# Optimization experiments

Measured on AMD Instinct MI355X. Metric: run time of the kernel, lower is better.

## Reference

```python
import jax, jax.numpy as jnp
import numpy as np

# Module hyperparameters (init_kwargs)
N_CLASSES = 21
RADIUS = 5
SIZE = (256, 256)
SIGMA_DIST = 4.0
SIGMA_FEAT = 1.0
B, C = 8, 32


def _offsets(radius):
    """Integer (dy, dx) offsets with Euclidean distance < radius (includes (0,0))."""
    offs = []
    r = int(radius)
    for dy in range(-r + 1, r):
        for dx in range(-r + 1, r):
            if dy * dy + dx * dx < radius * radius:
                offs.append((dy, dx))
    return offs


OFFSETS = _offsets(RADIUS)  # 69 offsets for radius=5


def setup_inputs() -> dict:
    key = jax.random.key(0)
    k1, k2 = jax.random.split(key)
    H, W = SIZE
    classification = jax.random.uniform(k1, (B, N_CLASSES, H, W), dtype=jnp.float32)
    features = jax.random.normal(k2, (B, C, H, W), dtype=jnp.float32)
    return {"classification": classification, "features": features}


def reference(classification, features):
    # classification: [B, K, H, W] soft assignments S
    # features:       [B, C, H, W]
    Bb, K, H, W = classification.shape
    inv_sd2 = 1.0 / (SIGMA_DIST * SIGMA_DIST)
    inv_sf2 = 1.0 / (SIGMA_FEAT * SIGMA_FEAT)

    hs = jnp.arange(H)
    ws = jnp.arange(W)

    WS = jnp.zeros_like(classification)           # (W @ S), [B, K, H, W]
    degree = jnp.zeros((Bb, H, W), classification.dtype)

    # Loop over the small fixed set of neighbor offsets (69 for radius=5).
    for dy, dx in OFFSETS:
        f_nb = jnp.roll(features, (-dy, -dx), axis=(2, 3))
        s_nb = jnp.roll(classification, (-dy, -dx), axis=(2, 3))
        # mask out wrap-around: neighbor (h+dy, w+dx) must be in-bounds
        valid_h = (hs + dy >= 0) & (hs + dy < H)
        valid_w = (ws + dx >= 0) & (ws + dx < W)
        mask = (valid_h[:, None] & valid_w[None, :]).astype(classification.dtype)
        # Gaussian affinity: distance kernel * feature kernel
        feat_d2 = ((features - f_nb) ** 2).sum(axis=1)        # [B, H, W]
        w = jnp.exp(-(dy * dy + dx * dx) * inv_sd2 - feat_d2 * inv_sf2) * mask
        WS = WS + w[:, None] * s_nb
        degree = degree + w

    # numerator   = S^T W S : [B, K, K]
    # denominator = d^T S   : [B, K]
    num = jnp.einsum('bkhw,bjhw->bkj', classification, WS)
    den = jnp.einsum('bhw,bkhw->bk', degree, classification)
    return (num / den[:, None, :]).sum()
```

## Files before the change

kernel.cpp:

```cpp
#include <hip/hip_runtime.h>

#define HH 256
#define WW 256
#define HWPX 65536
#define BB 8
#define KK 21
#define CC 32
#define NT 8192
#define E_LOG2E 1.4426950408889634f
#define PEN -30000.0f

typedef _Float16 half2v __attribute__((ext_vector_type(2)));
typedef _Float16 half8  __attribute__((ext_vector_type(8)));
typedef float    f32x4v __attribute__((ext_vector_type(4)));
union F4H { float4 f4; half2v h[4]; half8 h8; };

__global__ __launch_bounds__(256) void prep(const float* __restrict__ cls,
                                            const float* __restrict__ feat,
                                            float4* __restrict__ fpk,
                                            float2* __restrict__ TN,
                                            float* __restrict__ out) {
    const int tid = blockIdx.x * 256 + threadIdx.x;
    if (tid == 0) out[0] = 0.f;
    const int b = tid >> 16;
    const int p = tid & (HWPX - 1);

    const float* cbase = cls + (size_t)b * KK * HWPX + p;
    float T = 0.f;
#pragma unroll
    for (int k = 0; k < KK; ++k) T += cbase[(size_t)k * HWPX];

    const float* src = feat + (size_t)b * CC * HWPX + p;
    float nq = 0.f;
#pragma unroll
    for (int j = 0; j < 4; ++j) {
        F4H u;
#pragma unroll
        for (int k = 0; k < 4; ++k) {
            float a  = src[(size_t)(j * 8 + 2 * k) * HWPX];
            float b2 = src[(size_t)(j * 8 + 2 * k + 1) * HWPX];
            u.h[k] = __builtin_bit_cast(half2v, __builtin_amdgcn_cvt_pkrtz(a, b2));
            nq = __builtin_amdgcn_fdot2(u.h[k], u.h[k], nq, false);
        }
        fpk[(size_t)j * (BB * HWPX) + tid] = u.f4;
    }
    TN[tid] = make_float2(T, nq);
}

__global__ __launch_bounds__(256, 6) void affinity_mfma(const float4* __restrict__ fpk,
                                                        const float2* __restrict__ TN,
                                                        const float* __restrict__ cls,
                                                        float* __restrict__ partial) {
    __shared__ float smN[4][21], smD[4][21];
    const int L    = blockIdx.x;
    const int b    = L & 7;
    const int t    = L >> 3;
    const int wid  = threadIdx.x >> 6;
    const int lane = threadIdx.x & 63;
    const int g    = lane >> 4;
    const int c    = lane & 15;
    const int idx  = t * 4 + wid;
    const int y0   = (idx >> 5) * 2;
    const int x0   = (idx & 31) * 8;

    const size_t bofs = (size_t)b * HWPX;
    const float4* fb  = fpk + bofs;
    const float2* tnb = TN + bofs;

    F4H afr;
    afr.f4 = fb[(size_t)g * (BB * HWPX) + ((y0 + (c & 1)) << 8) + x0 + (c >> 1)];

    int pxr[4];
    float npE[4];
#pragma unroll
    for (int r = 0; r < 4; ++r) {
        pxr[r] = ((y0 + (r & 1)) << 8) + x0 + 2 * g + (r >> 1);
        npE[r] = tnb[pxr[r]].y * E_LOG2E;
    }

    const int xbu  = x0 - 4 + c;
    const bool inb = (unsigned)xbu < WW;
    const int xbc  = min(max(xbu, 0), WW - 1);
    const int voffF = (g * (BB * HWPX) + xbc) * 16;
    const int voffT = xbc * 8;

    float cstL16[4], cstL9[4], cstL4[4];
#pragma unroll
    for (int r = 0; r < 4; ++r) {
        const int dx = c - 4 - 2 * g - (r >> 1);
        const int s2 = dx * dx;
        const float bp = fmaf((float)s2, -E_LOG2E / 16.f, -npE[r]);
        cstL16[r] = (inb && s2 <= 16) ? bp : PEN;
        cstL9[r]  = (inb && s2 <= 9)  ? bp : PEN;
        cstL4[r]  = (inb && s2 <= 4)  ? bp : PEN;
    }

    const f32x4v czero = {0.f, 0.f, 0.f, 0.f};
    float pdeg[4] = {0.f, 0.f, 0.f, 0.f};
    float pV[4]   = {0.f, 0.f, 0.f, 0.f};

    const char* fpkB = (const char*)fpk + bofs * 16;
    const char* tnB  = (const char*)TN + bofs * 8;

    auto body = [&](int ny, const float (&ce)[4], const float (&co)[4],
                    float cdyE, float cdyO, int mode) {
        if ((unsigned)ny >= HH) return;
        const char* pF = fpkB + ((size_t)ny << 12);
        const char* pT = tnB  + ((size_t)ny << 11);
        F4H bfr; bfr.f4 = *(const float4*)(pF + voffF);
        const float2 tq = *(const float2*)(pT + voffT);
        f32x4v cz = __builtin_amdgcn_mfma_f32_16x16x32_f16(afr.h8, bfr.h8, czero, 0, 0, 0);
        if (mode != 2) {
            const float te = fmaf(tq.y, -E_LOG2E, cdyE);
            const float e0 = fmaf(cz[0], 2.f * E_LOG2E, ce[0] + te);
            const float w0 = __builtin_exp2f(e0);
            pdeg[0] += w0;  pV[0] = fmaf(w0, tq.x, pV[0]);
            const float e2 = fmaf(cz[2], 2.f * E_LOG2E, ce[2] + te);
            const float w2 = __builtin_exp2f(e2);
            pdeg[2] += w2;  pV[2] = fmaf(w2, tq.x, pV[2]);
        }
        if (mode != 1) {
            const float to = fmaf(tq.y, -E_LOG2E, cdyO);
            const float e1 = fmaf(cz[1], 2.f * E_LOG2E, co[1] + to);
            const float w1 = __builtin_exp2f(e1);
            pdeg[1] += w1;  pV[1] = fmaf(w1, tq.x, pV[1]);
            const float e3 = fmaf(cz[3], 2.f * E_LOG2E, co[3] + to);
            const float w3 = __builtin_exp2f(e3);
            pdeg[3] += w3;  pV[3] = fmaf(w3, tq.x, pV[3]);
        }
    };

#define CDY(D) ((float)(D) * (-E_LOG2E / 16.f))
    body(y0 - 4, cstL4,  cstL4,  CDY(16), CDY(16), 1);
    body(y0 - 3, cstL9,  cstL4,  CDY(9),  CDY(16), 0);
    body(y0 - 2, cstL16, cstL9,  CDY(4),  CDY(9),  0);
    body(y0 - 1, cstL16, cstL16, CDY(1),  CDY(4),  0);
    body(y0 + 0, cstL16, cstL16, CDY(0),  CDY(1),  0);
    body(y0 + 1, cstL16, cstL16, CDY(1),  CDY(0),  0);
    body(y0 + 2, cstL16, cstL16, CDY(4),  CDY(1),  0);
    body(y0 + 3, cstL9,  cstL16, CDY(9),  CDY(4),  0);
    body(y0 + 4, cstL4,  cstL9,  CDY(16), CDY(9),  0);
    body(y0 + 5, cstL4,  cstL4,  CDY(16), CDY(16), 2);
#undef CDY

#pragma unroll
    for (int m = 1; m <= 8; m <<= 1) {
#pragma unroll
        for (int r = 0; r < 4; ++r) {
            pdeg[r] += __shfl_xor(pdeg[r], m, 64);
            pV[r]   += __shfl_xor(pV[r], m, 64);
        }
    }

    float n0 = 0.f, d0 = 0.f, n1 = 0.f, d1 = 0.f;
    const float* clsb = cls + (size_t)b * KK * HWPX;
#pragma unroll
    for (int r = 0; r < 4; ++r) {
        const float s0 = clsb[(size_t)c * HWPX + pxr[r]];
        n0 = fmaf(s0, pV[r], n0);
        d0 = fmaf(s0, pdeg[r], d0);
        if (c < 5) {
            const float s1 = clsb[(size_t)(c + 16) * HWPX + pxr[r]];
            n1 = fmaf(s1, pV[r], n1);
            d1 = fmaf(s1, pdeg[r], d1);
        }
    }
#pragma unroll
    for (int m = 16; m <= 32; m <<= 1) {
        n0 += __shfl_xor(n0, m, 64);
        d0 += __shfl_xor(d0, m, 64);
        n1 += __shfl_xor(n1, m, 64);
        d1 += __shfl_xor(d1, m, 64);
    }
    if (lane < 16) {
        smN[wid][lane] = n0;
        smD[wid][lane] = d0;
        if (lane < 5) { smN[wid][16 + lane] = n1; smD[wid][16 + lane] = d1; }
    }
    __syncthreads();
    if (threadIdx.x < 2 * KK) {
        const int jq = threadIdx.x;
        const float v = (jq < KK)
            ? (smN[0][jq] + smN[1][jq] + smN[2][jq] + smN[3][jq])
            : (smD[0][jq - KK] + smD[1][jq - KK] + smD[2][jq - KK] + smD[3][jq - KK]);
        partial[(size_t)jq * NT + (size_t)b * 1024 + t] = v;
    }
}

__global__ __launch_bounds__(256) void reduce_fin(const float* __restrict__ partial,
                                                  float* __restrict__ out) {
    __shared__ float smn[4], smd[4];
    const int j = blockIdx.x;
    const int b = blockIdx.y;
    const float4 n4 = ((const float4*)(partial + (size_t)j        * NT + (size_t)b * 1024))[threadIdx.x];
    const float4 d4 = ((const float4*)(partial + (size_t)(j + KK) * NT + (size_t)b * 1024))[threadIdx.x];
    float n = (n4.x + n4.y) + (n4.z + n4.w);
    float d = (d4.x + d4.y) + (d4.z + d4.w);
#pragma unroll
    for (int off = 32; off > 0; off >>= 1) {
        n += __shfl_down(n, off);
        d += __shfl_down(d, off);
    }
    if ((threadIdx.x & 63) == 0) { smn[threadIdx.x >> 6] = n; smd[threadIdx.x >> 6] = d; }
    __syncthreads();
    if (threadIdx.x == 0) {
        const float N = (smn[0] + smn[1]) + (smn[2] + smn[3]);
        const float D = (smd[0] + smd[1]) + (smd[2] + smd[3]);
        atomicAdd(out, N / D);
    }
}

extern "C" void kernel_launch(void* const* d_in, const int* in_sizes, int n_in,
                              void* d_out, int out_size, void* d_ws, size_t ws_size,
                              hipStream_t stream) {
    const float* cls  = (const float*)d_in[0];
    const float* feat = (const float*)d_in[1];
    float* out = (float*)d_out;

    const size_t BHW = (size_t)BB * HWPX;
    float4* fpk     = (float4*)d_ws;
    float2* TN      = (float2*)((char*)d_ws + BHW * 64);
    float*  partial = (float*)((char*)TN + BHW * 8);

    prep<<<dim3((BB * HWPX) / 256), dim3(256), 0, stream>>>(cls, feat, fpk, TN, out);
    affinity_mfma<<<dim3(NT), dim3(256), 0, stream>>>(fpk, TN, cls, partial);
    reduce_fin<<<dim3(KK, BB), dim3(256), 0, stream>>>(partial, out);
}
```

Measured before the change: 179.4 us.

## Process two row-pairs per wave to reuse neighbor-row loads across tiles

Each wave now covers 4 rows instead of 2, holding two A fragments and running 12 neighbor-row windows in place of 2×10. Each loaded neighbor row (features and T/norm) feeds MFMAs for both tiles, which cuts the global loads for the halo rows. Grid size and partial-reduction layout are halved to match. The cost is more live registers (a second set of accumulators and constants), which may lower occupancy under the 6-wave launch bound.

```diff
diff --git a/kernel.cpp b/kernel.cpp
--- a/kernel.cpp
+++ b/kernel.cpp
@@ -6,7 +6,7 @@
 #define BB 8
 #define KK 21
 #define CC 32
-#define NT 8192
+#define NTB 4096
 #define E_LOG2E 1.4426950408889634f
 #define PEN -30000.0f
 
@@ -60,22 +60,24 @@
     const int g    = lane >> 4;
     const int c    = lane & 15;
     const int idx  = t * 4 + wid;
-    const int y0   = (idx >> 5) * 2;
+    const int y0   = (idx >> 5) * 4;
     const int x0   = (idx & 31) * 8;
 
     const size_t bofs = (size_t)b * HWPX;
     const float4* fb  = fpk + bofs;
     const float2* tnb = TN + bofs;
 
-    F4H afr;
-    afr.f4 = fb[(size_t)g * (BB * HWPX) + ((y0 + (c & 1)) << 8) + x0 + (c >> 1)];
-
-    int pxr[4];
-    float npE[4];
+    F4H afr0, afr1;
+    afr0.f4 = fb[(size_t)g * (BB * HWPX) + ((y0 + (c & 1)) << 8) + x0 + (c >> 1)];
+    afr1.f4 = fb[(size_t)g * (BB * HWPX) + ((y0 + 2 + (c & 1)) << 8) + x0 + (c >> 1)];
+
+    int pxr0[4];
+    float npE0[4], npE1[4];
 #pragma unroll
     for (int r = 0; r < 4; ++r) {
-        pxr[r] = ((y0 + (r & 1)) << 8) + x0 + 2 * g + (r >> 1);
-        npE[r] = tnb[pxr[r]].y * E_LOG2E;
+        pxr0[r] = ((y0 + (r & 1)) << 8) + x0 + 2 * g + (r >> 1);
+        npE0[r] = tnb[pxr0[r]].y * E_LOG2E;
+        npE1[r] = tnb[pxr0[r] + 512].y * E_LOG2E;
     }
 
     const int xbu  = x0 - 4 + c;
@@ -84,71 +86,89 @@
     const int voffF = (g * (BB * HWPX) + xbc) * 16;
     const int voffT = xbc * 8;
 
-    float cstL16[4], cstL9[4], cstL4[4];
+    float c16_0[4], c9_0[4], c4_0[4], c16_1[4], c9_1[4], c4_1[4];
 #pragma unroll
     for (int r = 0; r < 4; ++r) {
         const int dx = c - 4 - 2 * g - (r >> 1);
         const int s2 = dx * dx;
-        const float bp = fmaf((float)s2, -E_LOG2E / 16.f, -npE[r]);
-        cstL16[r] = (inb && s2 <= 16) ? bp : PEN;
-        cstL9[r]  = (inb && s2 <= 9)  ? bp : PEN;
-        cstL4[r]  = (inb && s2 <= 4)  ? bp : PEN;
+        const float bp0 = fmaf((float)s2, -E_LOG2E / 16.f, -npE0[r]);
+        const float bp1 = fmaf((float)s2, -E_LOG2E / 16.f, -npE1[r]);
+        c16_0[r] = (inb && s2 <= 16) ? bp0 : PEN;
+        c9_0[r]  = (inb && s2 <= 9)  ? bp0 : PEN;
+        c4_0[r]  = (inb && s2 <= 4)  ? bp0 : PEN;
+        c16_1[r] = (inb && s2 <= 16) ? bp1 : PEN;
+        c9_1[r]  = (inb && s2 <= 9)  ? bp1 : PEN;
+        c4_1[r]  = (inb && s2 <= 4)  ? bp1 : PEN;
     }
 
     const f32x4v czero = {0.f, 0.f, 0.f, 0.f};
-    float pdeg[4] = {0.f, 0.f, 0.f, 0.f};
-    float pV[4]   = {0.f, 0.f, 0.f, 0.f};
+    float pd0[4] = {0.f, 0.f, 0.f, 0.f}, pv0[4] = {0.f, 0.f, 0.f, 0.f};
+    float pd1[4] = {0.f, 0.f, 0.f, 0.f}, pv1[4] = {0.f, 0.f, 0.f, 0.f};
 
     const char* fpkB = (const char*)fpk + bofs * 16;
     const char* tnB  = (const char*)TN + bofs * 8;
 
-    auto body = [&](int ny, const float (&ce)[4], const float (&co)[4],
-                    float cdyE, float cdyO, int mode) {
-        if ((unsigned)ny >= HH) return;
-        const char* pF = fpkB + ((size_t)ny << 12);
-        const char* pT = tnB  + ((size_t)ny << 11);
-        F4H bfr; bfr.f4 = *(const float4*)(pF + voffF);
-        const float2 tq = *(const float2*)(pT + voffT);
+    auto tbody = [&](const F4H& bfr, const float2& tq, const F4H& afr,
+                     const float (&ce)[4], const float (&co)[4],
+                     float (&pd)[4], float (&pv)[4],
+                     float cdyE, float cdyO, int mode) {
         f32x4v cz = __builtin_amdgcn_mfma_f32_16x16x32_f16(afr.h8, bfr.h8, czero, 0, 0, 0);
         if (mode != 2) {
             const float te = fmaf(tq.y, -E_LOG2E, cdyE);
             const float e0 = fmaf(cz[0], 2.f * E_LOG2E, ce[0] + te);
             const float w0 = __builtin_exp2f(e0);
-            pdeg[0] += w0;  pV[0] = fmaf(w0, tq.x, pV[0]);
+            pd[0] += w0;  pv[0] = fmaf(w0, tq.x, pv[0]);
             const float e2 = fmaf(cz[2], 2.f * E_LOG2E, ce[2] + te);
             const float w2 = __builtin_exp2f(e2);
-            pdeg[2] += w2;  pV[2] = fmaf(w2, tq.x, pV[2]);
+            pd[2] += w2;  pv[2] = fmaf(w2, tq.x, pv[2]);
         }
         if (mode != 1) {
             const float to = fmaf(tq.y, -E_LOG2E, cdyO);
             const float e1 = fmaf(cz[1], 2.f * E_LOG2E, co[1] + to);
             const float w1 = __builtin_exp2f(e1);
-            pdeg[1] += w1;  pV[1] = fmaf(w1, tq.x, pV[1]);
+            pd[1] += w1;  pv[1] = fmaf(w1, tq.x, pv[1]);
             const float e3 = fmaf(cz[3], 2.f * E_LOG2E, co[3] + to);
             const float w3 = __builtin_exp2f(e3);
-            pdeg[3] += w3;  pV[3] = fmaf(w3, tq.x, pV[3]);
+            pd[3] += w3;  pv[3] = fmaf(w3, tq.x, pv[3]);
         }
     };
 
 #define CDY(D) ((float)(D) * (-E_LOG2E / 16.f))
-    body(y0 - 4, cstL4,  cstL4,  CDY(16), CDY(16), 1);
-    body(y0 - 3, cstL9,  cstL4,  CDY(9),  CDY(16), 0);
-    body(y0 - 2, cstL16, cstL9,  CDY(4),  CDY(9),  0);
-    body(y0 - 1, cstL16, cstL16, CDY(1),  CDY(4),  0);
-    body(y0 + 0, cstL16, cstL16, CDY(0),  CDY(1),  0);
-    body(y0 + 1, cstL16, cstL16, CDY(1),  CDY(0),  0);
-    body(y0 + 2, cstL16, cstL16, CDY(4),  CDY(1),  0);
-    body(y0 + 3, cstL9,  cstL16, CDY(9),  CDY(4),  0);
-    body(y0 + 4, cstL4,  cstL9,  CDY(16), CDY(9),  0);
-    body(y0 + 5, cstL4,  cstL4,  CDY(16), CDY(16), 2);
+#define WIN(I, T0ACT, CE0, CO0, DE0, DO0, M0, T1ACT, CE1, CO1, DE1, DO1, M1)              \
+    {                                                                                     \
+        const int ny = y0 - 4 + (I);                                                      \
+        if ((unsigned)ny < HH) {                                                          \
+            F4H bfr; float2 tq;                                                           \
+            bfr.f4 = *(const float4*)(fpkB + ((size_t)ny << 12) + voffF);                 \
+            tq     = *(const float2*)(tnB  + ((size_t)ny << 11) + voffT);                 \
+            if (T0ACT) tbody(bfr, tq, afr0, CE0, CO0, pd0, pv0, CDY(DE0), CDY(DO0), M0);  \
+            if (T1ACT) tbody(bfr, tq, afr1, CE1, CO1, pd1, pv1, CDY(DE1), CDY(DO1), M1);  \
+        }                                                                                 \
+    }
+
+    WIN(0,  1, c4_0,  c4_0,  16, 16, 1,   0, c4_1,  c4_1,  16, 16, 0)
+    WIN(1,  1, c9_0,  c4_0,   9, 16, 0,   0, c4_1,  c4_1,  16, 16, 0)
+    WIN(2,  1, c16_0, c9_0,   4,  9, 0,   1, c4_1,  c4_1,  16, 16, 1)
+    WIN(3,  1, c16_0, c16_0,  1,  4, 0,   1, c9_1,  c4_1,   9, 16, 0)
+    WIN(4,  1, c16_0, c16_0,  0,  1, 0,   1, c16_1, c9_1,   4,  9, 0)
+    WIN(5,  1, c16_0, c16_0,  1,  0, 0,   1, c16_1, c16_1,  1,  4, 0)
+    WIN(6,  1, c16_0, c16_0,  4,  1, 0,   1, c16_1, c16_1,  0,  1, 0)
+    WIN(7,  1, c9_0,  c16_0,  9,  4, 0,   1, c16_1, c16_1,  1,  0, 0)
+    WIN(8,  1, c4_0,  c9_0,  16,  9, 0,   1, c16_1, c16_1,  4,  1, 0)
+    WIN(9,  1, c4_0,  c4_0,  16, 16, 2,   1, c9_1,  c16_1,  9,  4, 0)
+    WIN(10, 0, c4_0,  c4_0,  16, 16, 0,   1, c4_1,  c9_1,  16,  9, 0)
+    WIN(11, 0, c4_0,  c4_0,  16, 16, 0,   1, c4_1,  c4_1,  16, 16, 2)
+#undef WIN
 #undef CDY
 
 #pragma unroll
     for (int m = 1; m <= 8; m <<= 1) {
 #pragma unroll
         for (int r = 0; r < 4; ++r) {
-            pdeg[r] += __shfl_xor(pdeg[r], m, 64);
-            pV[r]   += __shfl_xor(pV[r], m, 64);
+            pd0[r] += __shfl_xor(pd0[r], m, 64);
+            pv0[r] += __shfl_xor(pv0[r], m, 64);
+            pd1[r] += __shfl_xor(pd1[r], m, 64);
+            pv1[r] += __shfl_xor(pv1[r], m, 64);
         }
     }
 
@@ -156,13 +176,15 @@
     const float* clsb = cls + (size_t)b * KK * HWPX;
 #pragma unroll
     for (int r = 0; r < 4; ++r) {
-        const float s0 = clsb[(size_t)c * HWPX + pxr[r]];
-        n0 = fmaf(s0, pV[r], n0);
-        d0 = fmaf(s0, pdeg[r], d0);
+        const float s0a = clsb[(size_t)c * HWPX + pxr0[r]];
+        const float s0b = clsb[(size_t)c * HWPX + pxr0[r] + 512];
+        n0 = fmaf(s0a, pv0[r], n0);  n0 = fmaf(s0b, pv1[r], n0);
+        d0 = fmaf(s0a, pd0[r], d0);  d0 = fmaf(s0b, pd1[r], d0);
         if (c < 5) {
-            const float s1 = clsb[(size_t)(c + 16) * HWPX + pxr[r]];
-            n1 = fmaf(s1, pV[r], n1);
-            d1 = fmaf(s1, pdeg[r], d1);
+            const float s1a = clsb[(size_t)(c + 16) * HWPX + pxr0[r]];
+            const float s1b = clsb[(size_t)(c + 16) * HWPX + pxr0[r] + 512];
+            n1 = fmaf(s1a, pv0[r], n1);  n1 = fmaf(s1b, pv1[r], n1);
+            d1 = fmaf(s1a, pd0[r], d1);  d1 = fmaf(s1b, pd1[r], d1);
         }
     }
 #pragma unroll
@@ -183,7 +205,7 @@
         const float v = (jq < KK)
             ? (smN[0][jq] + smN[1][jq] + smN[2][jq] + smN[3][jq])
             : (smD[0][jq - KK] + smD[1][jq - KK] + smD[2][jq - KK] + smD[3][jq - KK]);
-        partial[(size_t)jq * NT + (size_t)b * 1024 + t] = v;
+        partial[(size_t)jq * NTB + (size_t)b * 512 + t] = v;
     }
 }
 
@@ -192,10 +214,10 @@
     __shared__ float smn[4], smd[4];
     const int j = blockIdx.x;
     const int b = blockIdx.y;
-    const float4 n4 = ((const float4*)(partial + (size_t)j        * NT + (size_t)b * 1024))[threadIdx.x];
-    const float4 d4 = ((const float4*)(partial + (size_t)(j + KK) * NT + (size_t)b * 1024))[threadIdx.x];
-    float n = (n4.x + n4.y) + (n4.z + n4.w);
-    float d = (d4.x + d4.y) + (d4.z + d4.w);
+    const float2 n2 = ((const float2*)(partial + (size_t)j        * NTB + (size_t)b * 512))[threadIdx.x];
+    const float2 d2 = ((const float2*)(partial + (size_t)(j + KK) * NTB + (size_t)b * 512))[threadIdx.x];
+    float n = n2.x + n2.y;
+    float d = d2.x + d2.y;
 #pragma unroll
     for (int off = 32; off > 0; off >>= 1) {
         n += __shfl_down(n, off);
@@ -223,6 +245,6 @@
     float*  partial = (float*)((char*)TN + BHW * 8);
 
     prep<<<dim3((BB * HWPX) / 256), dim3(256), 0, stream>>>(cls, feat, fpk, TN, out);
-    affinity_mfma<<<dim3(NT), dim3(256), 0, stream>>>(fpk, TN, cls, partial);
+    affinity_mfma<<<dim3(NTB), dim3(256), 0, stream>>>(fpk, TN, cls, partial);
     reduce_fin<<<dim3(KK, BB), dim3(256), 0, stream>>>(partial, out);
 }
```

New measurement: 175.0 us, median of 2. -2.5%, faster.

## Process four row-pairs per wave to reuse neighbor row loads across MFMAs

Applied to the files above, without the earlier changes.

Each wave now covers an 8-row by 8-column tile instead of 2x8, holding four A fragments and sweeping 16 neighbor rows once. Each loaded neighbor row feeds up to four MFMA/exp groups, which cuts redundant global loads of the halo rows (10 loads per 2 rows down to 16 per 8 rows). The grid shrinks fourfold and the occupancy hint is dropped, which raises register pressure (16 accumulators per array) and lowers parallelism.

```diff
diff --git a/kernel.cpp b/kernel.cpp
--- a/kernel.cpp
+++ b/kernel.cpp
@@ -6,7 +6,7 @@
 #define BB 8
 #define KK 21
 #define CC 32
-#define NT 8192
+#define NTB 2048
 #define E_LOG2E 1.4426950408889634f
 #define PEN -30000.0f
 
@@ -47,10 +47,10 @@
     TN[tid] = make_float2(T, nq);
 }
 
-__global__ __launch_bounds__(256, 6) void affinity_mfma(const float4* __restrict__ fpk,
-                                                        const float2* __restrict__ TN,
-                                                        const float* __restrict__ cls,
-                                                        float* __restrict__ partial) {
+__global__ __launch_bounds__(256) void affinity_mfma(const float4* __restrict__ fpk,
+                                                     const float2* __restrict__ TN,
+                                                     const float* __restrict__ cls,
+                                                     float* __restrict__ partial) {
     __shared__ float smN[4][21], smD[4][21];
     const int L    = blockIdx.x;
     const int b    = L & 7;
@@ -60,23 +60,22 @@
     const int g    = lane >> 4;
     const int c    = lane & 15;
     const int idx  = t * 4 + wid;
-    const int y0   = (idx >> 5) * 2;
+    const int y0   = (idx >> 5) * 8;
     const int x0   = (idx & 31) * 8;
 
     const size_t bofs = (size_t)b * HWPX;
     const float4* fb  = fpk + bofs;
     const float2* tnb = TN + bofs;
 
-    F4H afr;
-    afr.f4 = fb[(size_t)g * (BB * HWPX) + ((y0 + (c & 1)) << 8) + x0 + (c >> 1)];
+    F4H afr[4];
+#pragma unroll
+    for (int k = 0; k < 4; ++k)
+        afr[k].f4 = fb[(size_t)g * (BB * HWPX) + ((y0 + 2 * k + (c & 1)) << 8) + x0 + (c >> 1)];
 
     int pxr[4];
-    float npE[4];
-#pragma unroll
-    for (int r = 0; r < 4; ++r) {
+#pragma unroll
+    for (int r = 0; r < 4; ++r)
         pxr[r] = ((y0 + (r & 1)) << 8) + x0 + 2 * g + (r >> 1);
-        npE[r] = tnb[pxr[r]].y * E_LOG2E;
-    }
 
     const int xbu  = x0 - 4 + c;
     const bool inb = (unsigned)xbu < WW;
@@ -84,87 +83,99 @@
     const int voffF = (g * (BB * HWPX) + xbc) * 16;
     const int voffT = xbc * 8;
 
-    float cstL16[4], cstL9[4], cstL4[4];
-#pragma unroll
-    for (int r = 0; r < 4; ++r) {
-        const int dx = c - 4 - 2 * g - (r >> 1);
-        const int s2 = dx * dx;
-        const float bp = fmaf((float)s2, -E_LOG2E / 16.f, -npE[r]);
-        cstL16[r] = (inb && s2 <= 16) ? bp : PEN;
-        cstL9[r]  = (inb && s2 <= 9)  ? bp : PEN;
-        cstL4[r]  = (inb && s2 <= 4)  ? bp : PEN;
-    }
+    float cstB[4][4];
+    bool ok9[2], ok4[2];
+#pragma unroll
+    for (int h = 0; h < 2; ++h) {
+        const int dx = c - 4 - 2 * g - h;
+        ok9[h] = dx * dx <= 9;
+        ok4[h] = dx * dx <= 4;
+    }
+#pragma unroll
+    for (int k = 0; k < 4; ++k)
+#pragma unroll
+        for (int r = 0; r < 4; ++r) {
+            const int dx = c - 4 - 2 * g - (r >> 1);
+            const int s2 = dx * dx;
+            const float npE = tnb[pxr[r] + 512 * k].y * E_LOG2E;
+            cstB[k][r] = (inb && s2 <= 16) ? fmaf((float)s2, -E_LOG2E / 16.f, -npE) : PEN;
+        }
 
     const f32x4v czero = {0.f, 0.f, 0.f, 0.f};
-    float pdeg[4] = {0.f, 0.f, 0.f, 0.f};
-    float pV[4]   = {0.f, 0.f, 0.f, 0.f};
+    float pd[4][4], pv[4][4];
+#pragma unroll
+    for (int k = 0; k < 4; ++k)
+#pragma unroll
+        for (int r = 0; r < 4; ++r) { pd[k][r] = 0.f; pv[k][r] = 0.f; }
 
     const char* fpkB = (const char*)fpk + bofs * 16;
     const char* tnB  = (const char*)TN + bofs * 8;
 
-    auto body = [&](int ny, const float (&ce)[4], const float (&co)[4],
-                    float cdyE, float cdyO, int mode) {
-        if ((unsigned)ny >= HH) return;
-        const char* pF = fpkB + ((size_t)ny << 12);
-        const char* pT = tnB  + ((size_t)ny << 11);
-        F4H bfr; bfr.f4 = *(const float4*)(pF + voffF);
-        const float2 tq = *(const float2*)(pT + voffT);
-        f32x4v cz = __builtin_amdgcn_mfma_f32_16x16x32_f16(afr.h8, bfr.h8, czero, 0, 0, 0);
-        if (mode != 2) {
-            const float te = fmaf(tq.y, -E_LOG2E, cdyE);
-            const float e0 = fmaf(cz[0], 2.f * E_LOG2E, ce[0] + te);
-            const float w0 = __builtin_exp2f(e0);
-            pdeg[0] += w0;  pV[0] = fmaf(w0, tq.x, pV[0]);
-            const float e2 = fmaf(cz[2], 2.f * E_LOG2E, ce[2] + te);
-            const float w2 = __builtin_exp2f(e2);
-            pdeg[2] += w2;  pV[2] = fmaf(w2, tq.x, pV[2]);
-        }
-        if (mode != 1) {
-            const float to = fmaf(tq.y, -E_LOG2E, cdyO);
-            const float e1 = fmaf(cz[1], 2.f * E_LOG2E, co[1] + to);
-            const float w1 = __builtin_exp2f(e1);
-            pdeg[1] += w1;  pV[1] = fmaf(w1, tq.x, pV[1]);
-            const float e3 = fmaf(cz[3], 2.f * E_LOG2E, co[3] + to);
-            const float w3 = __builtin_exp2f(e3);
-            pdeg[3] += w3;  pV[3] = fmaf(w3, tq.x, pV[3]);
-        }
-    };
-
-#define CDY(D) ((float)(D) * (-E_LOG2E / 16.f))
-    body(y0 - 4, cstL4,  cstL4,  CDY(16), CDY(16), 1);
-    body(y0 - 3, cstL9,  cstL4,  CDY(9),  CDY(16), 0);
-    body(y0 - 2, cstL16, cstL9,  CDY(4),  CDY(9),  0);
-    body(y0 - 1, cstL16, cstL16, CDY(1),  CDY(4),  0);
-    body(y0 + 0, cstL16, cstL16, CDY(0),  CDY(1),  0);
-    body(y0 + 1, cstL16, cstL16, CDY(1),  CDY(0),  0);
-    body(y0 + 2, cstL16, cstL16, CDY(4),  CDY(1),  0);
-    body(y0 + 3, cstL9,  cstL16, CDY(9),  CDY(4),  0);
-    body(y0 + 4, cstL4,  cstL9,  CDY(16), CDY(9),  0);
-    body(y0 + 5, cstL4,  cstL4,  CDY(16), CDY(16), 2);
-#undef CDY
-
-#pragma unroll
-    for (int m = 1; m <= 8; m <<= 1) {
-#pragma unroll
-        for (int r = 0; r < 4; ++r) {
-            pdeg[r] += __shfl_xor(pdeg[r], m, 64);
-            pV[r]   += __shfl_xor(pV[r], m, 64);
-        }
-    }
+#define SEL(BASE, LIM, H) ((LIM) == 0 ? (BASE) : ((LIM) == 1 ? (ok9[H] ? (BASE) : PEN) \
+                                                             : (ok4[H] ? (BASE) : PEN)))
+
+#pragma unroll
+    for (int i = 0; i < 16; ++i) {
+        const int ny = y0 - 4 + i;
+        if ((unsigned)ny >= HH) continue;
+        F4H bfr; bfr.f4 = *(const float4*)(fpkB + ((size_t)ny << 12) + voffF);
+        const float2 tq = *(const float2*)(tnB  + ((size_t)ny << 11) + voffT);
+#pragma unroll
+        for (int k = 0; k < 4; ++k) {
+            if (i < 2 * k || i > 2 * k + 9) continue;
+            const int DE   = (i - 4 - 2 * k) * (i - 4 - 2 * k);
+            const int DO   = (i - 5 - 2 * k) * (i - 5 - 2 * k);
+            const int mode = (i == 2 * k) ? 1 : ((i == 2 * k + 9) ? 2 : 0);
+            const int limE = DE <= 4 ? 0 : (DE == 9 ? 1 : 2);
+            const int limO = DO <= 4 ? 0 : (DO == 9 ? 1 : 2);
+            f32x4v cz = __builtin_amdgcn_mfma_f32_16x16x32_f16(afr[k].h8, bfr.h8, czero, 0, 0, 0);
+            if (mode != 2) {
+                const float te = fmaf(tq.y, -E_LOG2E, (float)DE * (-E_LOG2E / 16.f));
+                const float e0 = fmaf(cz[0], 2.f * E_LOG2E, SEL(cstB[k][0], limE, 0) + te);
+                const float w0 = __builtin_exp2f(e0);
+                pd[k][0] += w0;  pv[k][0] = fmaf(w0, tq.x, pv[k][0]);
+                const float e2 = fmaf(cz[2], 2.f * E_LOG2E, SEL(cstB[k][2], limE, 1) + te);
+                const float w2 = __builtin_exp2f(e2);
+                pd[k][2] += w2;  pv[k][2] = fmaf(w2, tq.x, pv[k][2]);
+            }
+            if (mode != 1) {
+                const float to = fmaf(tq.y, -E_LOG2E, (float)DO * (-E_LOG2E / 16.f));
+                const float e1 = fmaf(cz[1], 2.f * E_LOG2E, SEL(cstB[k][1], limO, 0) + to);
+                const float w1 = __builtin_exp2f(e1);
+                pd[k][1] += w1;  pv[k][1] = fmaf(w1, tq.x, pv[k][1]);
+                const float e3 = fmaf(cz[3], 2.f * E_LOG2E, SEL(cstB[k][3], limO, 1) + to);
+                const float w3 = __builtin_exp2f(e3);
+                pd[k][3] += w3;  pv[k][3] = fmaf(w3, tq.x, pv[k][3]);
+            }
+        }
+    }
+#undef SEL
+
+#pragma unroll
+    for (int m = 1; m <= 8; m <<= 1)
+#pragma unroll
+        for (int k = 0; k < 4; ++k)
+#pragma unroll
+            for (int r = 0; r < 4; ++r) {
+                pd[k][r] += __shfl_xor(pd[k][r], m, 64);
+                pv[k][r] += __shfl_xor(pv[k][r], m, 64);
+            }
 
     float n0 = 0.f, d0 = 0.f, n1 = 0.f, d1 = 0.f;
     const float* clsb = cls + (size_t)b * KK * HWPX;
 #pragma unroll
-    for (int r = 0; r < 4; ++r) {
-        const float s0 = clsb[(size_t)c * HWPX + pxr[r]];
-        n0 = fmaf(s0, pV[r], n0);
-        d0 = fmaf(s0, pdeg[r], d0);
-        if (c < 5) {
-            const float s1 = clsb[(size_t)(c + 16) * HWPX + pxr[r]];
-            n1 = fmaf(s1, pV[r], n1);
-            d1 = fmaf(s1, pdeg[r], d1);
-        }
-    }
+    for (int r = 0; r < 4; ++r)
+#pragma unroll
+        for (int k = 0; k < 4; ++k) {
+            const float s0 = clsb[(size_t)c * HWPX + pxr[r] + 512 * k];
+            n0 = fmaf(s0, pv[k][r], n0);
+            d0 = fmaf(s0, pd[k][r], d0);
+            if (c < 5) {
+                const float s1 = clsb[(size_t)(c + 16) * HWPX + pxr[r] + 512 * k];
+                n1 = fmaf(s1, pv[k][r], n1);
+                d1 = fmaf(s1, pd[k][r], d1);
+            }
+        }
 #pragma unroll
     for (int m = 16; m <= 32; m <<= 1) {
         n0 += __shfl_xor(n0, m, 64);
@@ -183,7 +194,7 @@
         const float v = (jq < KK)
             ? (smN[0][jq] + smN[1][jq] + smN[2][jq] + smN[3][jq])
             : (smD[0][jq - KK] + smD[1][jq - KK] + smD[2][jq - KK] + smD[3][jq - KK]);
-        partial[(size_t)jq * NT + (size_t)b * 1024 + t] = v;
+        partial[(size_t)jq * NTB + (size_t)b * 256 + t] = v;
     }
 }
 
@@ -192,10 +203,8 @@
     __shared__ float smn[4], smd[4];
     const int j = blockIdx.x;
     const int b = blockIdx.y;
-    const float4 n4 = ((const float4*)(partial + (size_t)j        * NT + (size_t)b * 1024))[threadIdx.x];
-    const float4 d4 = ((const float4*)(partial + (size_t)(j + KK) * NT + (size_t)b * 1024))[threadIdx.x];
-    float n = (n4.x + n4.y) + (n4.z + n4.w);
-    float d = (d4.x + d4.y) + (d4.z + d4.w);
+    float n = partial[(size_t)j        * NTB + (size_t)b * 256 + threadIdx.x];
+    float d = partial[(size_t)(j + KK) * NTB + (size_t)b * 256 + threadIdx.x];
 #pragma unroll
     for (int off = 32; off > 0; off >>= 1) {
         n += __shfl_down(n, off);
@@ -223,6 +232,6 @@
     float*  partial = (float*)((char*)TN + BHW * 8);
 
     prep<<<dim3((BB * HWPX) / 256), dim3(256), 0, stream>>>(cls, feat, fpk, TN, out);
-    affinity_mfma<<<dim3(NT), dim3(256), 0, stream>>>(fpk, TN, cls, partial);
+    affinity_mfma<<<dim3(NTB), dim3(256), 0, stream>>>(fpk, TN, cls, partial);
     reduce_fin<<<dim3(KK, BB), dim3(256), 0, stream>>>(partial, out);
 }
```

Measured after the change: 183.8 us. 1.02x slower.
